# Optimization experiments

Measured on AMD Instinct MI355X. Metric: run time of the kernel, lower is better.

## Reference

```python
import jax, jax.numpy as jnp
import numpy as np

V = 50257       # vocab size (leaves of Huffman tree)
N_DEC = V - 1   # internal decision nodes
D = 1024        # input_size
N_EX = 8192     # number of examples (tokens)
MAX_LEN = 24    # max Huffman path depth


def setup_inputs() -> dict:
    key = jax.random.key(0)
    k_x, k_w, k_t, k_p, k_c, k_l = jax.random.split(key, 6)
    x = jax.random.normal(k_x, (N_EX, D), dtype=jnp.float32)
    W = jax.random.normal(k_w, (N_DEC, D), dtype=jnp.float32) * 0.02
    t = jax.random.randint(k_t, (N_EX,), 0, V, dtype=jnp.int32)
    # padded per-leaf tree paths: decision-node indices and +/-1 branch codes
    paths = jax.random.randint(k_p, (V, MAX_LEN), 0, N_DEC, dtype=jnp.int32)
    codes = jnp.where(jax.random.bernoulli(k_c, 0.5, (V, MAX_LEN)), 1.0, -1.0).astype(jnp.float32)
    lens = jax.random.randint(k_l, (V,), 1, MAX_LEN + 1, dtype=jnp.int32)
    return {"x": x, "W": W, "t": t, "paths": paths, "codes": codes, "lens": lens}


def reference(x, W, t, paths, codes, lens):
    # Per-example tree path: gather the decision nodes / codes for each target leaf.
    node_idx = paths[t]            # [N_EX, MAX_LEN] int32
    code = codes[t]                # [N_EX, MAX_LEN] +/-1
    mask = (jnp.arange(MAX_LEN)[None, :] < lens[t][:, None]).astype(x.dtype)  # [N_EX, MAX_LEN]
    # Irregular gather of W rows along each path, then per-step dot products.
    Wp = W[node_idx]               # [N_EX, MAX_LEN, D]
    wxy = code * jnp.einsum('nd,nld->nl', x, Wp)   # [N_EX, MAX_LEN]
    # Per-decision binary log-loss: log(1 + exp(-wxy)), masked to true path length.
    ls = jax.nn.softplus(-wxy) * mask
    return ls.sum()
```

## Files before the change

kernel.cpp:

```cpp
#include <hip/hip_runtime.h>
#include <math.h>

#define HS_D       1024
#define HS_MAXLEN  24
#define HS_PAIRS   12
#define HS_PF_OFF  (1u << 21)

__global__ __launch_bounds__(256) void hsm_prefetch_kernel(
    const float4* __restrict__ W4, int nW4,
    const float4* __restrict__ x4, int nx4,
    float* __restrict__ ws)
{
    const int tid    = blockIdx.x * blockDim.x + threadIdx.x;
    const int stride = gridDim.x * blockDim.x;
    float s = 0.0f;
    for (int i = tid; i < nW4; i += stride) {
        const float4 v = W4[i];
        s += v.x + v.y + v.z + v.w;
    }
    for (int i = tid; i < nx4; i += stride) {
        const float4 v = x4[i];
        s += v.x + v.y + v.z + v.w;
    }
    ws[HS_PF_OFF + tid] = s;
}

__global__ __launch_bounds__(256) void hsm_pair_kernel(
    const float* __restrict__ x,
    const float* __restrict__ W,
    const int*   __restrict__ t,
    const int*   __restrict__ paths,
    const float* __restrict__ codes,
    const int*   __restrict__ lens,
    float*       __restrict__ ws)
{
    const int tid  = threadIdx.x;
    const int lane = tid & 63;
    const int gw   = blockIdx.x * 4 + (tid >> 6);
    const int n    = gw / HS_PAIRS;
    const int p    = gw % HS_PAIRS;

    const int leaf = t[n];
    const int L    = lens[leaf];
    const int l0   = 2 * p;
    const int l1   = l0 + 1;
    if (l0 >= L) {
        if (lane == 0) ws[gw] = 0.0f;
        return;
    }

    const int   node0 = paths[leaf * HS_MAXLEN + l0];
    const float c0    = codes[leaf * HS_MAXLEN + l0];
    const bool  v1    = (l1 < L);
    const int   node1 = v1 ? paths[leaf * HS_MAXLEN + l1] : node0;
    const float c1    = v1 ? codes[leaf * HS_MAXLEN + l1] : 1.0f;

    const float4* w0 = (const float4*)(W + (size_t)node0 * HS_D);
    const float4* w1 = (const float4*)(W + (size_t)node1 * HS_D);
    const float4* x4 = (const float4*)(x + (size_t)n     * HS_D);

    float4 wf0[4], wf1[4], xf[4];
#pragma unroll
    for (int j = 0; j < 4; ++j) wf0[j] = w0[j * 64 + lane];
#pragma unroll
    for (int j = 0; j < 4; ++j) wf1[j] = w1[j * 64 + lane];
#pragma unroll
    for (int j = 0; j < 4; ++j) xf[j]  = x4[j * 64 + lane];

    float d0 = 0.0f, d1 = 0.0f;
#pragma unroll
    for (int j = 0; j < 4; ++j) {
        d0 += xf[j].x * wf0[j].x + xf[j].y * wf0[j].y
            + xf[j].z * wf0[j].z + xf[j].w * wf0[j].w;
        d1 += xf[j].x * wf1[j].x + xf[j].y * wf1[j].y
            + xf[j].z * wf1[j].z + xf[j].w * wf1[j].w;
    }

#pragma unroll
    for (int off = 32; off > 0; off >>= 1) {
        d0 += __shfl_down(d0, off);
        d1 += __shfl_down(d1, off);
    }

    if (lane == 0) {
        const float z0 = -c0 * d0;
        float v = fmaxf(z0, 0.0f) + log1pf(expf(-fabsf(z0)));
        if (v1) {
            const float z1 = -c1 * d1;
            v += fmaxf(z1, 0.0f) + log1pf(expf(-fabsf(z1)));
        }
        ws[gw] = v;
    }
}

__global__ __launch_bounds__(1024) void hsm_finish_kernel(
    const float* __restrict__ ws, int n_slots, float* __restrict__ out)
{
    const int tid = threadIdx.x;
    float s = 0.0f;
    for (int i = tid; i < n_slots; i += 1024)
        s += ws[i];
#pragma unroll
    for (int off = 32; off > 0; off >>= 1)
        s += __shfl_down(s, off);
    __shared__ float sred[16];
    if ((tid & 63) == 0) sred[tid >> 6] = s;
    __syncthreads();
    if (tid == 0) {
        float tot = 0.0f;
#pragma unroll
        for (int w = 0; w < 16; ++w) tot += sred[w];
        out[0] = tot;
    }
}

extern "C" void kernel_launch(void* const* d_in, const int* in_sizes, int n_in,
                              void* d_out, int out_size, void* d_ws, size_t ws_size,
                              hipStream_t stream) {
    const float* x     = (const float*)d_in[0];
    const float* W     = (const float*)d_in[1];
    const int*   t     = (const int*)  d_in[2];
    const int*   paths = (const int*)  d_in[3];
    const float* codes = (const float*)d_in[4];
    const int*   lens  = (const int*)  d_in[5];
    float* out = (float*)d_out;
    float* ws  = (float*)d_ws;

    const int n_ex = in_sizes[2];
    const int nW4  = in_sizes[1] / 4;
    const int nx4  = in_sizes[0] / 4;

    hsm_prefetch_kernel<<<4096, 256, 0, stream>>>(
        (const float4*)W, nW4, (const float4*)x, nx4, ws);

    const int n_waves  = n_ex * HS_PAIRS;
    const int n_blocks = (n_waves + 3) / 4;
    hsm_pair_kernel<<<n_blocks, 256, 0, stream>>>(x, W, t, paths, codes, lens, ws);

    hsm_finish_kernel<<<1, 1024, 0, stream>>>(ws, n_waves, out);
}
```

Before: 397.2 us.

## Drop L2 prefetch kernel and process four path steps per wave

Removes the separate prefetch kernel that streamed all of W and x to warm the cache before the main work. Each wave now handles four path steps (l0, l0+1, l0+12, l0+13) instead of two, so the x row is loaded once for four dot products, and the number of waves is halved. Loads for steps past the path length are skipped. The trade-off is more registers per wave and losing the cache warming, so first-touch W gathers now hit HBM directly.

```diff
diff --git a/kernel.cpp b/kernel.cpp
--- a/kernel.cpp
+++ b/kernel.cpp
@@ -1,31 +1,11 @@
 #include <hip/hip_runtime.h>
 #include <math.h>
 
-#define HS_D       1024
-#define HS_MAXLEN  24
-#define HS_PAIRS   12
-#define HS_PF_OFF  (1u << 21)
+#define HS_D      1024
+#define HS_MAXLEN 24
+#define HS_QPW    6
 
-__global__ __launch_bounds__(256) void hsm_prefetch_kernel(
-    const float4* __restrict__ W4, int nW4,
-    const float4* __restrict__ x4, int nx4,
-    float* __restrict__ ws)
-{
-    const int tid    = blockIdx.x * blockDim.x + threadIdx.x;
-    const int stride = gridDim.x * blockDim.x;
-    float s = 0.0f;
-    for (int i = tid; i < nW4; i += stride) {
-        const float4 v = W4[i];
-        s += v.x + v.y + v.z + v.w;
-    }
-    for (int i = tid; i < nx4; i += stride) {
-        const float4 v = x4[i];
-        s += v.x + v.y + v.z + v.w;
-    }
-    ws[HS_PF_OFF + tid] = s;
-}
-
-__global__ __launch_bounds__(256) void hsm_pair_kernel(
+__global__ __launch_bounds__(256, 4) void hsm_quad_kernel(
     const float* __restrict__ x,
     const float* __restrict__ W,
     const int*   __restrict__ t,
@@ -36,58 +16,97 @@
 {
     const int tid  = threadIdx.x;
     const int lane = tid & 63;
-    const int gw   = blockIdx.x * 4 + (tid >> 6);
-    const int n    = gw / HS_PAIRS;
-    const int p    = gw % HS_PAIRS;
+    const int wv   = __builtin_amdgcn_readfirstlane(tid >> 6);
+    const int gw   = blockIdx.x * 4 + wv;
+    const int n    = gw / HS_QPW;
+    const int q    = gw % HS_QPW;
 
     const int leaf = t[n];
     const int L    = lens[leaf];
-    const int l0   = 2 * p;
-    const int l1   = l0 + 1;
+
+    const int l0 = 2 * q;
     if (l0 >= L) {
         if (lane == 0) ws[gw] = 0.0f;
         return;
     }
+    const bool v1 = (l0 + 1)  < L;
+    const bool v2 = (l0 + 12) < L;
+    const bool v3 = (l0 + 13) < L;
 
-    const int   node0 = paths[leaf * HS_MAXLEN + l0];
-    const float c0    = codes[leaf * HS_MAXLEN + l0];
-    const bool  v1    = (l1 < L);
-    const int   node1 = v1 ? paths[leaf * HS_MAXLEN + l1] : node0;
-    const float c1    = v1 ? codes[leaf * HS_MAXLEN + l1] : 1.0f;
+    const int base = leaf * HS_MAXLEN + l0;
+    const int   nd0 = paths[base];      const float cd0 = codes[base];
+    const int   nd1 = paths[base + 1];  const float cd1 = codes[base + 1];
+    const int   nd2 = paths[base + 12]; const float cd2 = codes[base + 12];
+    const int   nd3 = paths[base + 13]; const float cd3 = codes[base + 13];
 
-    const float4* w0 = (const float4*)(W + (size_t)node0 * HS_D);
-    const float4* w1 = (const float4*)(W + (size_t)node1 * HS_D);
-    const float4* x4 = (const float4*)(x + (size_t)n     * HS_D);
+    const float4* w0 = (const float4*)(W + (size_t)nd0 * HS_D);
+    const float4* w1 = (const float4*)(W + (size_t)nd1 * HS_D);
+    const float4* w2 = (const float4*)(W + (size_t)nd2 * HS_D);
+    const float4* w3 = (const float4*)(W + (size_t)nd3 * HS_D);
+    const float4* x4 = (const float4*)(x + (size_t)n   * HS_D);
 
-    float4 wf0[4], wf1[4], xf[4];
+    float4 wf0[4], wf1[4], wf2[4], wf3[4], xf[4];
 #pragma unroll
     for (int j = 0; j < 4; ++j) wf0[j] = w0[j * 64 + lane];
+    if (v1) {
 #pragma unroll
-    for (int j = 0; j < 4; ++j) wf1[j] = w1[j * 64 + lane];
+        for (int j = 0; j < 4; ++j) wf1[j] = w1[j * 64 + lane];
+    } else {
 #pragma unroll
-    for (int j = 0; j < 4; ++j) xf[j]  = x4[j * 64 + lane];
+        for (int j = 0; j < 4; ++j) wf1[j] = make_float4(0.f, 0.f, 0.f, 0.f);
+    }
+    if (v2) {
+#pragma unroll
+        for (int j = 0; j < 4; ++j) wf2[j] = w2[j * 64 + lane];
+    } else {
+#pragma unroll
+        for (int j = 0; j < 4; ++j) wf2[j] = make_float4(0.f, 0.f, 0.f, 0.f);
+    }
+    if (v3) {
+#pragma unroll
+        for (int j = 0; j < 4; ++j) wf3[j] = w3[j * 64 + lane];
+    } else {
+#pragma unroll
+        for (int j = 0; j < 4; ++j) wf3[j] = make_float4(0.f, 0.f, 0.f, 0.f);
+    }
+#pragma unroll
+    for (int j = 0; j < 4; ++j) xf[j] = x4[j * 64 + lane];
 
-    float d0 = 0.0f, d1 = 0.0f;
+    float d0 = 0.f, d1 = 0.f, d2 = 0.f, d3 = 0.f;
 #pragma unroll
     for (int j = 0; j < 4; ++j) {
         d0 += xf[j].x * wf0[j].x + xf[j].y * wf0[j].y
             + xf[j].z * wf0[j].z + xf[j].w * wf0[j].w;
         d1 += xf[j].x * wf1[j].x + xf[j].y * wf1[j].y
             + xf[j].z * wf1[j].z + xf[j].w * wf1[j].w;
+        d2 += xf[j].x * wf2[j].x + xf[j].y * wf2[j].y
+            + xf[j].z * wf2[j].z + xf[j].w * wf2[j].w;
+        d3 += xf[j].x * wf3[j].x + xf[j].y * wf3[j].y
+            + xf[j].z * wf3[j].z + xf[j].w * wf3[j].w;
     }
 
 #pragma unroll
     for (int off = 32; off > 0; off >>= 1) {
         d0 += __shfl_down(d0, off);
         d1 += __shfl_down(d1, off);
+        d2 += __shfl_down(d2, off);
+        d3 += __shfl_down(d3, off);
     }
 
     if (lane == 0) {
-        const float z0 = -c0 * d0;
-        float v = fmaxf(z0, 0.0f) + log1pf(expf(-fabsf(z0)));
+        const float z0 = -cd0 * d0;
+        float v = fmaxf(z0, 0.f) + log1pf(expf(-fabsf(z0)));
         if (v1) {
-            const float z1 = -c1 * d1;
-            v += fmaxf(z1, 0.0f) + log1pf(expf(-fabsf(z1)));
+            const float z1 = -cd1 * d1;
+            v += fmaxf(z1, 0.f) + log1pf(expf(-fabsf(z1)));
+        }
+        if (v2) {
+            const float z2 = -cd2 * d2;
+            v += fmaxf(z2, 0.f) + log1pf(expf(-fabsf(z2)));
+        }
+        if (v3) {
+            const float z3 = -cd3 * d3;
+            v += fmaxf(z3, 0.f) + log1pf(expf(-fabsf(z3)));
         }
         ws[gw] = v;
     }
@@ -126,16 +145,10 @@
     float* out = (float*)d_out;
     float* ws  = (float*)d_ws;
 
-    const int n_ex = in_sizes[2];
-    const int nW4  = in_sizes[1] / 4;
-    const int nx4  = in_sizes[0] / 4;
+    const int n_ex    = in_sizes[2];
+    const int n_waves = n_ex * HS_QPW;
+    const int n_blocks = (n_waves + 3) / 4;
 
-    hsm_prefetch_kernel<<<4096, 256, 0, stream>>>(
-        (const float4*)W, nW4, (const float4*)x, nx4, ws);
-
-    const int n_waves  = n_ex * HS_PAIRS;
-    const int n_blocks = (n_waves + 3) / 4;
-    hsm_pair_kernel<<<n_blocks, 256, 0, stream>>>(x, W, t, paths, codes, lens, ws);
-
+    hsm_quad_kernel<<<n_blocks, 256, 0, stream>>>(x, W, t, paths, codes, lens, ws);
     hsm_finish_kernel<<<1, 1024, 0, stream>>>(ws, n_waves, out);
 }
```

Result: faster. 335.4 us (-15.6%).
